# Optimization experiments

Measured on AMD Instinct MI355X. Metric: run time of the kernel, lower is better.

The kernel has to match this reference:

```python
import jax, jax.numpy as jnp
import numpy as np

MAX_DEPTH = 8
LMBDA = 0.1
OUTPUT_DIM = 128


def setup_inputs() -> dict:
    key = jax.random.key(0)
    k1, k2, k3, k4, k5, k6 = jax.random.split(key, 6)
    B, D, C = 8192, 2048, OUTPUT_DIM
    n_inner = 2 ** MAX_DEPTH - 1  # 255 inner nodes, BFS order
    n_leaf = 2 ** MAX_DEPTH       # 256 leaves
    x = jax.random.normal(k1, (B, D), dtype=jnp.float32)
    target = jax.random.randint(k2, (B,), 0, C)
    # small scale so sigmoid gates are not saturated (log(pen), log(1-pen) finite)
    W = jax.random.normal(k3, (n_inner, D), dtype=jnp.float32) * 0.02
    b = jax.random.normal(k4, (n_inner,), dtype=jnp.float32) * 0.02
    beta = jax.random.normal(k5, (n_inner,), dtype=jnp.float32)
    leaf_params = jax.random.normal(k6, (n_leaf, C), dtype=jnp.float32)
    return {"x": x, "target": target, "W": W, "b": b, "beta": beta,
            "leaf_params": leaf_params}


def reference(x, target, W, b, beta, leaf_params):
    B = x.shape[0]
    C = leaf_params.shape[1]
    y = jax.nn.one_hot(target, C, dtype=x.dtype)  # target_onehot

    # All inner-node gates as one batched GEMM: p[b,i] = sigmoid(beta_i*(x@w_i+b_i))
    p = jax.nn.sigmoid(beta[None, :] * (x @ W.T + b[None, :]))  # [B, n_inner]

    # Level-by-level path probability propagation (BFS node order).
    path = jnp.ones((B, 1), x.dtype)
    penalties = []  # per-level [2^d] node penalties
    start = 0
    for d in range(MAX_DEPTH):
        n = 2 ** d
        p_lvl = p[:, start:start + n]                      # [B, 2^d]
        pen = jnp.sum(p_lvl * path, axis=0) / jnp.sum(path, axis=0)
        penalties.append(pen)
        # left child gets path*(1-p), right gets path*p; interleave -> next level
        path = jnp.stack([path * (1.0 - p_lvl), path * p_lvl], axis=-1).reshape(B, 2 * n)
        start += n
    # path: [B, n_leaf] leaf path probabilities (left-to-right order)

    Q = jax.nn.softmax(leaf_params, axis=-1)               # [n_leaf, C]
    TQ = y @ jnp.log(Q).T                                  # [B, n_leaf], y . log Q per leaf
    loss = jnp.mean(jnp.sum(path * TQ, axis=1))

    # Penalty C: only inner nodes whose children are NOT leaves contribute
    # (original get_penalty drops depth==max_depth nodes), depths 1..max_depth-1.
    Cpen = jnp.asarray(0.0, x.dtype)
    for d in range(MAX_DEPTH - 1):
        lam = LMBDA * 2.0 ** (-(d + 1))
        pen = penalties[d]
        Cpen = Cpen - lam * 0.5 * jnp.sum(jnp.log(pen) + jnp.log(1.0 - pen))

    total = -loss + Cpen

    # output: Q of the max-path-prob leaf per sample
    leaf_idx = jnp.argmax(path, axis=1)                    # [B]
    output = Q[leaf_idx]                                   # [B, C]
    return total, output
```

## Files before the change

kernel.cpp:

```cpp
#include <hip/hip_runtime.h>
#include <hip/hip_bf16.h>
#include <hip/hip_fp16.h>
#include <stdint.h>

#define B_SIZE 8192
#define D_SIZE 2048
#define C_SIZE 128
#define N_INNER 255
#define N_LEAF 256
#define NPAD 256
#define NBLK_PATH 512

typedef _Float16 half8 __attribute__((ext_vector_type(8)));
typedef __fp16 pk16x2 __attribute__((ext_vector_type(2)));
typedef float f32x4 __attribute__((ext_vector_type(4)));
typedef unsigned short u16;

__device__ inline uint32_t pkh(float a, float b) {
    pk16x2 h = __builtin_amdgcn_cvt_pkrtz(a, b);
    return __builtin_bit_cast(uint32_t, h);
}
__device__ inline void split4(const float4 v, uint2& hi, uint2& lo) {
    pk16x2 a01 = __builtin_amdgcn_cvt_pkrtz(v.x, v.y);
    pk16x2 a23 = __builtin_amdgcn_cvt_pkrtz(v.z, v.w);
    float r0 = v.x - (float)a01[0];
    float r1 = v.y - (float)a01[1];
    float r2 = v.z - (float)a23[0];
    float r3 = v.w - (float)a23[1];
    hi = make_uint2(__builtin_bit_cast(uint32_t, a01), __builtin_bit_cast(uint32_t, a23));
    lo = make_uint2(pkh(r0, r1), pkh(r2, r3));
}

__global__ __launch_bounds__(256) void prep_kernel(
    const float* __restrict__ Wsrc, u16* __restrict__ Wh, u16* __restrict__ Wl,
    const float* __restrict__ lp, float* __restrict__ Q, float* __restrict__ logQt)
{
    int bid = blockIdx.x;
    int t = threadIdx.x;
    if (bid < 256) {
        int row = bid;
        int k = t * 8;
        uint2 h0, l0, h1, l1;
        if (row < N_INNER) {
            float4 v0 = *(const float4*)(Wsrc + (size_t)row * D_SIZE + k);
            float4 v1 = *(const float4*)(Wsrc + (size_t)row * D_SIZE + k + 4);
            split4(v0, h0, l0); split4(v1, h1, l1);
        } else {
            h0 = l0 = h1 = l1 = make_uint2(0u, 0u);
        }
        *(uint2*)&Wh[(size_t)row * D_SIZE + k]     = h0;
        *(uint2*)&Wh[(size_t)row * D_SIZE + k + 4] = h1;
        *(uint2*)&Wl[(size_t)row * D_SIZE + k]     = l0;
        *(uint2*)&Wl[(size_t)row * D_SIZE + k + 4] = l1;
    } else {
        int row = bid - 256;
        __shared__ float red[128];
        float v = 0.f;
        if (t < 128) { v = lp[row * C_SIZE + t]; red[t] = v; }
        __syncthreads();
        for (int s = 64; s > 0; s >>= 1) { if (t < s) red[t] = fmaxf(red[t], red[t + s]); __syncthreads(); }
        float mx = red[0]; __syncthreads();
        float e = 0.f;
        if (t < 128) { e = expf(v - mx); red[t] = e; }
        __syncthreads();
        for (int s = 64; s > 0; s >>= 1) { if (t < s) red[t] += red[t + s]; __syncthreads(); }
        float sum = red[0];
        if (t < 128) {
            Q[row * C_SIZE + t] = e / sum;
            logQt[(size_t)t * N_LEAF + row] = (v - mx) - logf(sum);
        }
    }
}

#define GBM 64
#define GBK 32
#define GKSPLIT 4
#define KCHUNK (D_SIZE / GKSPLIT)
#define KITERS (KCHUNK / GBK)
#define LDKA 40

__global__ __launch_bounds__(256, 2) void gemm_mfma(
    const float* __restrict__ x, const u16* __restrict__ Wh, const u16* __restrict__ Wl,
    float* __restrict__ zp)
{
    __shared__ __align__(16) u16 sAh[4][GBM * LDKA];
    __shared__ __align__(16) u16 sAl[4][GBM * LDKA];

    const int t = threadIdx.x;
    const int lane = t & 63, w = t >> 6;
    const int lr = lane & 15, lq = lane >> 4;
    const int m0 = blockIdx.x * GBM;
    const int kz = blockIdx.z;
    const int kb0 = kz * KCHUNK;

    f32x4 acc[4][4];
    #pragma unroll
    for (int mt = 0; mt < 4; ++mt)
        #pragma unroll
        for (int nt = 0; nt < 4; ++nt) acc[mt][nt] = (f32x4){0.f, 0.f, 0.f, 0.f};

    float4 av_c[8];
    #pragma unroll
    for (int i = 0; i < 8; ++i) {
        int idx = i * 64 + lane;
        int row = idx >> 3, ch = idx & 7;
        av_c[i] = *(const float4*)(x + (size_t)(m0 + row) * D_SIZE + kb0 + ch * 4);
    }

    #pragma unroll
    for (int kt = 0; kt < KITERS; ++kt) {
        const int kb = kb0 + kt * GBK;
        half8 bh[4], bl[4];
        #pragma unroll
        for (int nt = 0; nt < 4; ++nt) {
            int row = w * 64 + nt * 16 + lr;
            bh[nt] = *(const half8*)(Wh + (size_t)row * D_SIZE + kb + lq * 8);
            bl[nt] = *(const half8*)(Wl + (size_t)row * D_SIZE + kb + lq * 8);
        }
        float4 av_n[8];
        if (kt + 1 < KITERS) {
            #pragma unroll
            for (int i = 0; i < 8; ++i) {
                int idx = i * 64 + lane;
                int row = idx >> 3, ch = idx & 7;
                av_n[i] = *(const float4*)(x + (size_t)(m0 + row) * D_SIZE + kb + GBK + ch * 4);
            }
        }
        #pragma unroll
        for (int i = 0; i < 8; ++i) {
            int idx = i * 64 + lane;
            int row = idx >> 3, ch = idx & 7;
            uint2 hi, lo; split4(av_c[i], hi, lo);
            *(uint2*)&sAh[w][row * LDKA + ch * 4] = hi;
            *(uint2*)&sAl[w][row * LDKA + ch * 4] = lo;
        }
        asm volatile("s_waitcnt lgkmcnt(0)" ::: "memory");
        half8 ah[4], al[4];
        #pragma unroll
        for (int mt = 0; mt < 4; ++mt) {
            int off = (mt * 16 + lr) * LDKA + lq * 8;
            ah[mt] = *(const half8*)&sAh[w][off];
            al[mt] = *(const half8*)&sAl[w][off];
        }
        #pragma unroll
        for (int mt = 0; mt < 4; ++mt)
            #pragma unroll
            for (int nt = 0; nt < 4; ++nt) {
                acc[mt][nt] = __builtin_amdgcn_mfma_f32_16x16x32_f16(ah[mt], bh[nt], acc[mt][nt], 0, 0, 0);
                acc[mt][nt] = __builtin_amdgcn_mfma_f32_16x16x32_f16(ah[mt], bl[nt], acc[mt][nt], 0, 0, 0);
                acc[mt][nt] = __builtin_amdgcn_mfma_f32_16x16x32_f16(al[mt], bh[nt], acc[mt][nt], 0, 0, 0);
            }
        if (kt + 1 < KITERS) {
            #pragma unroll
            for (int i = 0; i < 8; ++i) av_c[i] = av_n[i];
        }
    }

    float* zout = zp + (size_t)kz * B_SIZE * NPAD;
    #pragma unroll
    for (int mt = 0; mt < 4; ++mt) {
        #pragma unroll
        for (int nt = 0; nt < 4; ++nt) {
            int gn = w * 64 + nt * 16 + lr;
            #pragma unroll
            for (int r = 0; r < 4; ++r) {
                int gm = m0 + mt * 16 + lq * 4 + r;
                zout[(size_t)gm * NPAD + gn] = acc[mt][nt][r];
            }
        }
    }
}

__global__ __launch_bounds__(256) void path_kernel(
    const float* __restrict__ z, const int* __restrict__ target,
    const float* __restrict__ bvec, const float* __restrict__ beta,
    const float* __restrict__ Q, const float* __restrict__ logQt,
    float* __restrict__ partial, float* __restrict__ out)
{
    __shared__ float pbuf[4][256];
    __shared__ float s_num[128], s_den[128], s_loss;
    const int t = threadIdx.x, w = t >> 6, lane = t & 63;
    const int c0 = lane * 4;
    float pnum[4] = {0.f, 0.f, 0.f, 0.f};
    float pden[4] = {0.f, 0.f, 0.f, 0.f};
    float loss = 0.f;

    if (t < 128) s_num[t] = 0.f;
    else s_den[t - 128] = 0.f;
    if (t == 0) s_loss = 0.f;
    __syncthreads();

    float bet[4], bia[4];
    #pragma unroll
    for (int j = 0; j < 4; ++j) {
        int c = c0 + j;
        bet[j] = (c < N_INNER) ? beta[c] : 0.f;
        bia[j] = (c < N_INNER) ? bvec[c] : 0.f;
    }

    for (int i = 0; i < 4; ++i) {
        int r = blockIdx.x * 16 + w * 4 + i;
        float4 s = make_float4(0.f, 0.f, 0.f, 0.f);
        #pragma unroll
        for (int p = 0; p < GKSPLIT; ++p) {
            float4 v = *(const float4*)(z + ((size_t)p * B_SIZE + r) * NPAD + c0);
            s.x += v.x; s.y += v.y; s.z += v.z; s.w += v.w;
        }
        float zv[4] = {s.x, s.y, s.z, s.w};
        float pv[4];
        #pragma unroll
        for (int j = 0; j < 4; ++j) {
            int c = c0 + j;
            pv[j] = (c < N_INNER) ? 1.f / (1.f + expf(-bet[j] * (zv[j] + bia[j]))) : 0.f;
        }
        *(float4*)&pbuf[w][c0] = make_float4(pv[0], pv[1], pv[2], pv[3]);
        asm volatile("s_waitcnt lgkmcnt(0)" ::: "memory");

        int tg = target[r];
        float4 lq4 = *(const float4*)(logQt + (size_t)tg * N_LEAF + c0);
        float lqa[4] = {lq4.x, lq4.y, lq4.z, lq4.w};
        float lsum = 0.f, bestV = -1.f;
        int bestI = 0;
        #pragma unroll
        for (int j = 0; j < 4; ++j) {
            int leaf = c0 + j;
            float pl = 1.f;
            #pragma unroll
            for (int d = 0; d < 8; ++d) {
                int node = (1 << d) - 1 + (leaf >> (8 - d));
                int bit = (leaf >> (7 - d)) & 1;
                float pvn = pbuf[w][node];
                pl *= bit ? pvn : (1.f - pvn);
            }
            lsum += pl * lqa[j];
            if (pl > bestV) { bestV = pl; bestI = leaf; }
        }
        if (lane < 32) {
            #pragma unroll
            for (int j = 0; j < 4; ++j) {
                int c = c0 + j;
                if (c < 127) {
                    int h = c + 1; int d = 31 - __clz(h);
                    float pp = 1.f;
                    for (int e = 0; e < d; ++e) {
                        int ha = h >> (d - e);
                        int bit = (h >> (d - 1 - e)) & 1;
                        float pvn = pbuf[w][ha - 1];
                        pp *= bit ? pvn : (1.f - pvn);
                    }
                    pnum[j] += pbuf[w][c] * pp;
                    pden[j] += pp;
                }
            }
        }
        #pragma unroll
        for (int m = 1; m < 64; m <<= 1) {
            lsum += __shfl_xor(lsum, m, 64);
            float ov = __shfl_xor(bestV, m, 64);
            int   oi = __shfl_xor(bestI, m, 64);
            if (ov > bestV || (ov == bestV && oi < bestI)) { bestV = ov; bestI = oi; }
        }
        loss += lsum;
        out[1 + (size_t)r * C_SIZE + lane]      = Q[bestI * C_SIZE + lane];
        out[1 + (size_t)r * C_SIZE + lane + 64] = Q[bestI * C_SIZE + lane + 64];
        asm volatile("" ::: "memory");
    }

    if (lane < 32) {
        #pragma unroll
        for (int j = 0; j < 4; ++j) {
            int c = c0 + j;
            if (c < 127) {
                atomicAdd(&s_num[c], pnum[j]);
                atomicAdd(&s_den[c], pden[j]);
            }
        }
    }
    if (lane == 0) atomicAdd(&s_loss, loss);
    __syncthreads();
    float* rec = partial + (size_t)blockIdx.x * 256;
    if (t < 127)        rec[t] = s_num[t];
    else if (t == 127)  rec[127] = s_loss;
    else if (t < 255)   rec[t] = s_den[t - 128];
    else                rec[255] = 0.f;
}

__global__ __launch_bounds__(256) void reduce_kernel(
    const float* __restrict__ partial, float* __restrict__ out)
{
    __shared__ float s[256];
    __shared__ float red[128];
    int t = threadIdx.x;
    float a0 = 0.f, a1 = 0.f, a2 = 0.f, a3 = 0.f;
    for (int r = 0; r < NBLK_PATH; r += 4) {
        a0 += partial[(size_t)(r + 0) * 256 + t];
        a1 += partial[(size_t)(r + 1) * 256 + t];
        a2 += partial[(size_t)(r + 2) * 256 + t];
        a3 += partial[(size_t)(r + 3) * 256 + t];
    }
    s[t] = (a0 + a1) + (a2 + a3);
    __syncthreads();
    float term = 0.f;
    if (t < 127) {
        int d = 31 - __clz(t + 1);
        float lam = 0.1f * exp2f(-(float)(d + 1));
        float pen = s[t] / s[128 + t];
        term = lam * 0.5f * (logf(pen) + logf(1.f - pen));
    }
    if (t < 128) { red[t] = term; }
    __syncthreads();
    for (int sh = 64; sh > 0; sh >>= 1) { if (t < sh) red[t] += red[t + sh]; __syncthreads(); }
    if (t == 0) out[0] = -(s[127] / (float)B_SIZE) - red[0];
}

extern "C" void kernel_launch(void* const* d_in, const int* in_sizes, int n_in,
                              void* d_out, int out_size, void* d_ws, size_t ws_size,
                              hipStream_t stream)
{
    const float* x    = (const float*)d_in[0];
    const int*   tgt  = (const int*)d_in[1];
    const float* W    = (const float*)d_in[2];
    const float* b    = (const float*)d_in[3];
    const float* beta = (const float*)d_in[4];
    const float* lp   = (const float*)d_in[5];
    float* out = (float*)d_out;

    float* z     = (float*)d_ws;
    float* Q     = z + (size_t)GKSPLIT * B_SIZE * NPAD;
    float* logQt = Q + (size_t)N_LEAF * C_SIZE;
    u16*   Wh    = (u16*)(logQt + (size_t)C_SIZE * N_LEAF);
    u16*   Wl    = Wh + (size_t)N_LEAF * D_SIZE;
    float* partial = (float*)(Wl + (size_t)N_LEAF * D_SIZE);

    prep_kernel<<<512, 256, 0, stream>>>(W, Wh, Wl, lp, Q, logQt);

    dim3 ggrid(B_SIZE / GBM, 1, GKSPLIT);
    gemm_mfma<<<ggrid, 256, 0, stream>>>(x, Wh, Wl, z);

    path_kernel<<<NBLK_PATH, 256, 0, stream>>>(
        z, tgt, b, beta, Q, logQt, partial, out);

    reduce_kernel<<<1, 256, 0, stream>>>(partial, out);
}
```

Baseline: 180.8 us.

## Load x fragments directly into MFMA layout and prefetch W into registers

The GEMM no longer stages x through per-wave LDS buffers. Each lane loads the 8 consecutive fp32 values it needs for the MFMA A-operand straight from global memory and splits them into hi/lo fp16 in registers. The W hi/lo fragments are now double-buffered in registers, so the next k-step's loads overlap the current MFMAs. This removes LDS writes, reads and waits, at the cost of more registers and global loads that are less coalesced (32-byte chunks per row).

```diff
diff --git a/kernel.cpp b/kernel.cpp
--- a/kernel.cpp
+++ b/kernel.cpp
@@ -29,6 +29,25 @@
     float r3 = v.w - (float)a23[1];
     hi = make_uint2(__builtin_bit_cast(uint32_t, a01), __builtin_bit_cast(uint32_t, a23));
     lo = make_uint2(pkh(r0, r1), pkh(r2, r3));
+}
+__device__ inline void split8(const float4 v0, const float4 v1, half8& hi8, half8& lo8) {
+    pk16x2 a01 = __builtin_amdgcn_cvt_pkrtz(v0.x, v0.y);
+    pk16x2 a23 = __builtin_amdgcn_cvt_pkrtz(v0.z, v0.w);
+    pk16x2 a45 = __builtin_amdgcn_cvt_pkrtz(v1.x, v1.y);
+    pk16x2 a67 = __builtin_amdgcn_cvt_pkrtz(v1.z, v1.w);
+    float r0 = v0.x - (float)a01[0];
+    float r1 = v0.y - (float)a01[1];
+    float r2 = v0.z - (float)a23[0];
+    float r3 = v0.w - (float)a23[1];
+    float r4 = v1.x - (float)a45[0];
+    float r5 = v1.y - (float)a45[1];
+    float r6 = v1.z - (float)a67[0];
+    float r7 = v1.w - (float)a67[1];
+    uint4 h = make_uint4(__builtin_bit_cast(uint32_t, a01), __builtin_bit_cast(uint32_t, a23),
+                         __builtin_bit_cast(uint32_t, a45), __builtin_bit_cast(uint32_t, a67));
+    uint4 l = make_uint4(pkh(r0, r1), pkh(r2, r3), pkh(r4, r5), pkh(r6, r7));
+    hi8 = __builtin_bit_cast(half8, h);
+    lo8 = __builtin_bit_cast(half8, l);
 }
 
 __global__ __launch_bounds__(256) void prep_kernel(
@@ -77,15 +96,11 @@
 #define GKSPLIT 4
 #define KCHUNK (D_SIZE / GKSPLIT)
 #define KITERS (KCHUNK / GBK)
-#define LDKA 40
 
 __global__ __launch_bounds__(256, 2) void gemm_mfma(
     const float* __restrict__ x, const u16* __restrict__ Wh, const u16* __restrict__ Wl,
     float* __restrict__ zp)
 {
-    __shared__ __align__(16) u16 sAh[4][GBM * LDKA];
-    __shared__ __align__(16) u16 sAl[4][GBM * LDKA];
-
     const int t = threadIdx.x;
     const int lane = t & 63, w = t >> 6;
     const int lr = lane & 15, lq = lane >> 4;
@@ -99,49 +114,45 @@
         #pragma unroll
         for (int nt = 0; nt < 4; ++nt) acc[mt][nt] = (f32x4){0.f, 0.f, 0.f, 0.f};
 
-    float4 av_c[8];
-    #pragma unroll
-    for (int i = 0; i < 8; ++i) {
-        int idx = i * 64 + lane;
-        int row = idx >> 3, ch = idx & 7;
-        av_c[i] = *(const float4*)(x + (size_t)(m0 + row) * D_SIZE + kb0 + ch * 4);
+    const float* xa = x + (size_t)(m0 + lr) * D_SIZE + kb0 + lq * 8;
+    const u16*   wh = Wh + (size_t)(w * 64 + lr) * D_SIZE + kb0 + lq * 8;
+    const u16*   wl = Wl + (size_t)(w * 64 + lr) * D_SIZE + kb0 + lq * 8;
+
+    float4 a0[4], a1[4];
+    half8 bh[4], bl[4];
+    #pragma unroll
+    for (int mt = 0; mt < 4; ++mt) {
+        const float* p = xa + (size_t)mt * 16 * D_SIZE;
+        a0[mt] = *(const float4*)(p);
+        a1[mt] = *(const float4*)(p + 4);
+    }
+    #pragma unroll
+    for (int nt = 0; nt < 4; ++nt) {
+        bh[nt] = *(const half8*)(wh + (size_t)nt * 16 * D_SIZE);
+        bl[nt] = *(const half8*)(wl + (size_t)nt * 16 * D_SIZE);
     }
 
     #pragma unroll
     for (int kt = 0; kt < KITERS; ++kt) {
-        const int kb = kb0 + kt * GBK;
-        half8 bh[4], bl[4];
-        #pragma unroll
-        for (int nt = 0; nt < 4; ++nt) {
-            int row = w * 64 + nt * 16 + lr;
-            bh[nt] = *(const half8*)(Wh + (size_t)row * D_SIZE + kb + lq * 8);
-            bl[nt] = *(const half8*)(Wl + (size_t)row * D_SIZE + kb + lq * 8);
-        }
-        float4 av_n[8];
+        float4 na0[4], na1[4];
+        half8 nbh[4], nbl[4];
         if (kt + 1 < KITERS) {
-            #pragma unroll
-            for (int i = 0; i < 8; ++i) {
-                int idx = i * 64 + lane;
-                int row = idx >> 3, ch = idx & 7;
-                av_n[i] = *(const float4*)(x + (size_t)(m0 + row) * D_SIZE + kb + GBK + ch * 4);
-            }
-        }
-        #pragma unroll
-        for (int i = 0; i < 8; ++i) {
-            int idx = i * 64 + lane;
-            int row = idx >> 3, ch = idx & 7;
-            uint2 hi, lo; split4(av_c[i], hi, lo);
-            *(uint2*)&sAh[w][row * LDKA + ch * 4] = hi;
-            *(uint2*)&sAl[w][row * LDKA + ch * 4] = lo;
-        }
-        asm volatile("s_waitcnt lgkmcnt(0)" ::: "memory");
+            const int ko = (kt + 1) * GBK;
+            #pragma unroll
+            for (int mt = 0; mt < 4; ++mt) {
+                const float* p = xa + (size_t)mt * 16 * D_SIZE + ko;
+                na0[mt] = *(const float4*)(p);
+                na1[mt] = *(const float4*)(p + 4);
+            }
+            #pragma unroll
+            for (int nt = 0; nt < 4; ++nt) {
+                nbh[nt] = *(const half8*)(wh + (size_t)nt * 16 * D_SIZE + ko);
+                nbl[nt] = *(const half8*)(wl + (size_t)nt * 16 * D_SIZE + ko);
+            }
+        }
         half8 ah[4], al[4];
         #pragma unroll
-        for (int mt = 0; mt < 4; ++mt) {
-            int off = (mt * 16 + lr) * LDKA + lq * 8;
-            ah[mt] = *(const half8*)&sAh[w][off];
-            al[mt] = *(const half8*)&sAl[w][off];
-        }
+        for (int mt = 0; mt < 4; ++mt) split8(a0[mt], a1[mt], ah[mt], al[mt]);
         #pragma unroll
         for (int mt = 0; mt < 4; ++mt)
             #pragma unroll
@@ -152,7 +163,9 @@
             }
         if (kt + 1 < KITERS) {
             #pragma unroll
-            for (int i = 0; i < 8; ++i) av_c[i] = av_n[i];
+            for (int mt = 0; mt < 4; ++mt) { a0[mt] = na0[mt]; a1[mt] = na1[mt]; }
+            #pragma unroll
+            for (int nt = 0; nt < 4; ++nt) { bh[nt] = nbh[nt]; bl[nt] = nbl[nt]; }
         }
     }
 
```

New measurement: 199.8 us. +10.5%, slower.

## Share A tile across 8 waves with double-buffered LDS and fuse final reduction

Applied to the files above, without the earlier changes.

The GEMM block grows to 512 threads arranged as 2x4 waves. The split-fp16 A tile is built once per block in shared memory and double-buffered, where before each wave built its own private copy. B fragments are prefetched one k-step ahead in registers. The separate reduce kernel is removed: the last path block, found through a global atomic counter, does the final reduction and resets the counter. This cuts redundant x loads and fp16 conversions and drops one launch, at the cost of a block-wide barrier on every k-step.

```diff
diff --git a/kernel.cpp b/kernel.cpp
--- a/kernel.cpp
+++ b/kernel.cpp
@@ -15,6 +15,8 @@
 typedef __fp16 pk16x2 __attribute__((ext_vector_type(2)));
 typedef float f32x4 __attribute__((ext_vector_type(4)));
 typedef unsigned short u16;
+
+__device__ unsigned int g_path_done = 0;
 
 __device__ inline uint32_t pkh(float a, float b) {
     pk16x2 h = __builtin_amdgcn_cvt_pkrtz(a, b);
@@ -79,92 +81,95 @@
 #define KITERS (KCHUNK / GBK)
 #define LDKA 40
 
-__global__ __launch_bounds__(256, 2) void gemm_mfma(
+__global__ __launch_bounds__(512, 4) void gemm_mfma(
     const float* __restrict__ x, const u16* __restrict__ Wh, const u16* __restrict__ Wl,
     float* __restrict__ zp)
 {
-    __shared__ __align__(16) u16 sAh[4][GBM * LDKA];
-    __shared__ __align__(16) u16 sAl[4][GBM * LDKA];
+    __shared__ __align__(16) u16 sAh[2][GBM * LDKA];
+    __shared__ __align__(16) u16 sAl[2][GBM * LDKA];
 
     const int t = threadIdx.x;
     const int lane = t & 63, w = t >> 6;
     const int lr = lane & 15, lq = lane >> 4;
+    const int wm = w >> 2, wn = w & 3;
     const int m0 = blockIdx.x * GBM;
     const int kz = blockIdx.z;
     const int kb0 = kz * KCHUNK;
 
-    f32x4 acc[4][4];
-    #pragma unroll
-    for (int mt = 0; mt < 4; ++mt)
+    const int arow = t >> 3, ach = t & 7;
+    const float* aptr = x + (size_t)(m0 + arow) * D_SIZE + kb0 + ach * 4;
+    const int sidx = arow * LDKA + ach * 4;
+
+    f32x4 acc[2][4];
+    #pragma unroll
+    for (int mt = 0; mt < 2; ++mt)
         #pragma unroll
         for (int nt = 0; nt < 4; ++nt) acc[mt][nt] = (f32x4){0.f, 0.f, 0.f, 0.f};
 
-    float4 av_c[8];
-    #pragma unroll
-    for (int i = 0; i < 8; ++i) {
-        int idx = i * 64 + lane;
-        int row = idx >> 3, ch = idx & 7;
-        av_c[i] = *(const float4*)(x + (size_t)(m0 + row) * D_SIZE + kb0 + ch * 4);
-    }
+    float4 areg = *(const float4*)aptr;
+    { uint2 hi, lo; split4(areg, hi, lo);
+      *(uint2*)&sAh[0][sidx] = hi;
+      *(uint2*)&sAl[0][sidx] = lo; }
+    areg = *(const float4*)(aptr + GBK);
+
+    half8 bh[4], bl[4];
+    #pragma unroll
+    for (int nt = 0; nt < 4; ++nt) {
+        const size_t ro = (size_t)(wn * 64 + nt * 16 + lr) * D_SIZE + kb0 + lq * 8;
+        bh[nt] = *(const half8*)(Wh + ro);
+        bl[nt] = *(const half8*)(Wl + ro);
+    }
+    __syncthreads();
 
     #pragma unroll
     for (int kt = 0; kt < KITERS; ++kt) {
-        const int kb = kb0 + kt * GBK;
-        half8 bh[4], bl[4];
-        #pragma unroll
-        for (int nt = 0; nt < 4; ++nt) {
-            int row = w * 64 + nt * 16 + lr;
-            bh[nt] = *(const half8*)(Wh + (size_t)row * D_SIZE + kb + lq * 8);
-            bl[nt] = *(const half8*)(Wl + (size_t)row * D_SIZE + kb + lq * 8);
-        }
-        float4 av_n[8];
+        const int cur = kt & 1;
+        half8 nbh[4], nbl[4];
         if (kt + 1 < KITERS) {
             #pragma unroll
-            for (int i = 0; i < 8; ++i) {
-                int idx = i * 64 + lane;
-                int row = idx >> 3, ch = idx & 7;
-                av_n[i] = *(const float4*)(x + (size_t)(m0 + row) * D_SIZE + kb + GBK + ch * 4);
-            }
-        }
-        #pragma unroll
-        for (int i = 0; i < 8; ++i) {
-            int idx = i * 64 + lane;
-            int row = idx >> 3, ch = idx & 7;
-            uint2 hi, lo; split4(av_c[i], hi, lo);
-            *(uint2*)&sAh[w][row * LDKA + ch * 4] = hi;
-            *(uint2*)&sAl[w][row * LDKA + ch * 4] = lo;
-        }
-        asm volatile("s_waitcnt lgkmcnt(0)" ::: "memory");
-        half8 ah[4], al[4];
-        #pragma unroll
-        for (int mt = 0; mt < 4; ++mt) {
-            int off = (mt * 16 + lr) * LDKA + lq * 8;
-            ah[mt] = *(const half8*)&sAh[w][off];
-            al[mt] = *(const half8*)&sAl[w][off];
-        }
-        #pragma unroll
-        for (int mt = 0; mt < 4; ++mt)
+            for (int nt = 0; nt < 4; ++nt) {
+                const size_t ro = (size_t)(wn * 64 + nt * 16 + lr) * D_SIZE + kb0 + (kt + 1) * GBK + lq * 8;
+                nbh[nt] = *(const half8*)(Wh + ro);
+                nbl[nt] = *(const half8*)(Wl + ro);
+            }
+        }
+        half8 ah[2], al[2];
+        #pragma unroll
+        for (int mt = 0; mt < 2; ++mt) {
+            const int off = (wm * 32 + mt * 16 + lr) * LDKA + lq * 8;
+            ah[mt] = *(const half8*)&sAh[cur][off];
+            al[mt] = *(const half8*)&sAl[cur][off];
+        }
+        if (kt + 1 < KITERS) {
+            uint2 hi, lo; split4(areg, hi, lo);
+            *(uint2*)&sAh[cur ^ 1][sidx] = hi;
+            *(uint2*)&sAl[cur ^ 1][sidx] = lo;
+            if (kt + 2 < KITERS) areg = *(const float4*)(aptr + (kt + 2) * GBK);
+        }
+        #pragma unroll
+        for (int mt = 0; mt < 2; ++mt)
             #pragma unroll
             for (int nt = 0; nt < 4; ++nt) {
                 acc[mt][nt] = __builtin_amdgcn_mfma_f32_16x16x32_f16(ah[mt], bh[nt], acc[mt][nt], 0, 0, 0);
                 acc[mt][nt] = __builtin_amdgcn_mfma_f32_16x16x32_f16(ah[mt], bl[nt], acc[mt][nt], 0, 0, 0);
                 acc[mt][nt] = __builtin_amdgcn_mfma_f32_16x16x32_f16(al[mt], bh[nt], acc[mt][nt], 0, 0, 0);
             }
+        __syncthreads();
         if (kt + 1 < KITERS) {
             #pragma unroll
-            for (int i = 0; i < 8; ++i) av_c[i] = av_n[i];
+            for (int nt = 0; nt < 4; ++nt) { bh[nt] = nbh[nt]; bl[nt] = nbl[nt]; }
         }
     }
 
     float* zout = zp + (size_t)kz * B_SIZE * NPAD;
     #pragma unroll
-    for (int mt = 0; mt < 4; ++mt) {
+    for (int mt = 0; mt < 2; ++mt) {
         #pragma unroll
         for (int nt = 0; nt < 4; ++nt) {
-            int gn = w * 64 + nt * 16 + lr;
+            int gn = wn * 64 + nt * 16 + lr;
             #pragma unroll
             for (int r = 0; r < 4; ++r) {
-                int gm = m0 + mt * 16 + lq * 4 + r;
+                int gm = m0 + wm * 32 + mt * 16 + lq * 4 + r;
                 zout[(size_t)gm * NPAD + gn] = acc[mt][nt][r];
             }
         }
@@ -179,6 +184,7 @@
 {
     __shared__ float pbuf[4][256];
     __shared__ float s_num[128], s_den[128], s_loss;
+    __shared__ int s_last;
     const int t = threadIdx.x, w = t >> 6, lane = t & 63;
     const int c0 = lane * 4;
     float pnum[4] = {0.f, 0.f, 0.f, 0.f};
@@ -283,34 +289,41 @@
     else if (t == 127)  rec[127] = s_loss;
     else if (t < 255)   rec[t] = s_den[t - 128];
     else                rec[255] = 0.f;
-}
-
-__global__ __launch_bounds__(256) void reduce_kernel(
-    const float* __restrict__ partial, float* __restrict__ out)
-{
-    __shared__ float s[256];
-    __shared__ float red[128];
-    int t = threadIdx.x;
-    float a0 = 0.f, a1 = 0.f, a2 = 0.f, a3 = 0.f;
-    for (int r = 0; r < NBLK_PATH; r += 4) {
-        a0 += partial[(size_t)(r + 0) * 256 + t];
-        a1 += partial[(size_t)(r + 1) * 256 + t];
-        a2 += partial[(size_t)(r + 2) * 256 + t];
-        a3 += partial[(size_t)(r + 3) * 256 + t];
-    }
-    s[t] = (a0 + a1) + (a2 + a3);
+
+    __threadfence();
+    if (t == 0) {
+        unsigned int prev = atomicAdd(&g_path_done, 1u);
+        s_last = (prev == NBLK_PATH - 1) ? 1 : 0;
+    }
     __syncthreads();
-    float term = 0.f;
-    if (t < 127) {
-        int d = 31 - __clz(t + 1);
-        float lam = 0.1f * exp2f(-(float)(d + 1));
-        float pen = s[t] / s[128 + t];
-        term = lam * 0.5f * (logf(pen) + logf(1.f - pen));
-    }
-    if (t < 128) { red[t] = term; }
-    __syncthreads();
-    for (int sh = 64; sh > 0; sh >>= 1) { if (t < sh) red[t] += red[t + sh]; __syncthreads(); }
-    if (t == 0) out[0] = -(s[127] / (float)B_SIZE) - red[0];
+    if (s_last) {
+        __threadfence();
+        __shared__ float fs[256];
+        __shared__ float fred[128];
+        float a0 = 0.f, a1 = 0.f, a2 = 0.f, a3 = 0.f;
+        for (int r2 = 0; r2 < NBLK_PATH; r2 += 4) {
+            a0 += partial[(size_t)(r2 + 0) * 256 + t];
+            a1 += partial[(size_t)(r2 + 1) * 256 + t];
+            a2 += partial[(size_t)(r2 + 2) * 256 + t];
+            a3 += partial[(size_t)(r2 + 3) * 256 + t];
+        }
+        fs[t] = (a0 + a1) + (a2 + a3);
+        __syncthreads();
+        float term = 0.f;
+        if (t < 127) {
+            int d = 31 - __clz(t + 1);
+            float lam = 0.1f * exp2f(-(float)(d + 1));
+            float pen = fs[t] / fs[128 + t];
+            term = lam * 0.5f * (logf(pen) + logf(1.f - pen));
+        }
+        if (t < 128) { fred[t] = term; }
+        __syncthreads();
+        for (int sh = 64; sh > 0; sh >>= 1) { if (t < sh) fred[t] += fred[t + sh]; __syncthreads(); }
+        if (t == 0) {
+            out[0] = -(fs[127] / (float)B_SIZE) - fred[0];
+            g_path_done = 0;
+        }
+    }
 }
 
 extern "C" void kernel_launch(void* const* d_in, const int* in_sizes, int n_in,
@@ -335,10 +348,8 @@
     prep_kernel<<<512, 256, 0, stream>>>(W, Wh, Wl, lp, Q, logQt);
 
     dim3 ggrid(B_SIZE / GBM, 1, GKSPLIT);
-    gemm_mfma<<<ggrid, 256, 0, stream>>>(x, Wh, Wl, z);
+    gemm_mfma<<<ggrid, 512, 0, stream>>>(x, Wh, Wl, z);
 
     path_kernel<<<NBLK_PATH, 256, 0, stream>>>(
         z, tgt, b, beta, Q, logQt, partial, out);
-
-    reduce_kernel<<<1, 256, 0, stream>>>(partial, out);
-}
+}
```

Measured after the change: 240.2 us. +32.9%, slower.
